# Kernel tuning notes

Hardware: AMD Instinct MI355X
Metric: run time of the kernel (lower is better)

## Reference

```python
import jax, jax.numpy as jnp
import numpy as np

H = 1024      # hidden_size
F = 1024      # intermediate_size
E = 8         # num_experts
K = 2         # num_experts_per_tok
B, S = 1, 2048


def setup_inputs() -> dict:
    key = jax.random.key(0)
    ks = jax.random.split(key, 8)
    s = 0.02
    return {
        "hidden_states": jax.random.normal(ks[0], (B, S, H), jnp.float32),
        "w_gate": jax.random.normal(ks[1], (H, E), jnp.float32) * s,
        "w_gate_proj": jax.random.normal(ks[2], (E, H, F), jnp.float32) * s,   # per-expert gate_proj
        "w_up_proj": jax.random.normal(ks[3], (E, H, F), jnp.float32) * s,     # per-expert up_proj
        "w_down_proj": jax.random.normal(ks[4], (E, F, H), jnp.float32) * s,   # per-expert down_proj
        "w_shared_gate": jax.random.normal(ks[5], (H, F), jnp.float32) * s,
        "w_shared_up": jax.random.normal(ks[6], (H, F), jnp.float32) * s,
        "w_shared_down": jax.random.normal(ks[7], (F, H), jnp.float32) * s,
    }


def reference(hidden_states, w_gate, w_gate_proj, w_up_proj, w_down_proj,
              w_shared_gate, w_shared_up, w_shared_down):
    b, s, h = hidden_states.shape
    x = hidden_states.reshape(-1, h)                       # [T, H]
    t = x.shape[0]

    # --- router ---
    router_logits = x @ w_gate                             # [T, E]
    topk_vals, topk_idx = jax.lax.top_k(router_logits, K)  # [T, K]
    expert_weights = jax.nn.softmax(topk_vals.astype(jnp.float32), axis=-1).astype(x.dtype)

    # dense per-token per-expert combine weight [T, E] (zero where not selected)
    combine = jnp.zeros((t, E), x.dtype).at[jnp.arange(t)[:, None], topk_idx].add(expert_weights)

    # --- all experts as one grouped GEMM (weight-zero experts contribute 0) ---
    g = jnp.einsum('th,ehf->tef', x, w_gate_proj)          # [T, E, F]
    u = jnp.einsum('th,ehf->tef', x, w_up_proj)            # [T, E, F]
    y = jnp.einsum('tef,efh->teh', jax.nn.silu(g) * u, w_down_proj)  # [T, E, H]
    out = jnp.einsum('teh,te->th', y, combine)             # [T, H]

    # --- shared expert ---
    shared = (jax.nn.silu(x @ w_shared_gate) * (x @ w_shared_up)) @ w_shared_down
    out = (out + shared).reshape(b, s, h)

    aux_loss = jnp.float32(0.0)
    return out, aux_loss
```

## Files before the change

kernel.cpp:

```cpp
#include <hip/hip_runtime.h>
#include <hip/hip_bf16.h>
#include <stdint.h>

#define HDIM 1024
#define FDIM 1024
#define TTOK 2048
#define CAP  2048
#define MSZ  (1024*1024)

typedef __attribute__((ext_vector_type(8))) __bf16 bf16x8;
typedef __attribute__((ext_vector_type(4))) float  f32x4;

static __device__ __forceinline__ unsigned short f2bf(float v) {
  unsigned int u = __float_as_uint(v);
  u += 0x7FFF + ((u >> 16) & 1);
  return (unsigned short)(u >> 16);
}

static __device__ __forceinline__ unsigned pk2(float a, float b) {
  return (unsigned)f2bf(a) | ((unsigned)f2bf(b) << 16);
}

static __device__ __forceinline__ void gload_lds16(const void* g, void* l) {
  __builtin_amdgcn_global_load_lds(
      (const __attribute__((address_space(1))) unsigned int*)g,
      (__attribute__((address_space(3))) unsigned int*)l, 16, 0, 0);
}

__global__ __launch_bounds__(256) void k_prep(
    const float* __restrict__ x, const float* __restrict__ wg,
    const float* __restrict__ wgp, const float* __restrict__ wsg,
    const float* __restrict__ wup, const float* __restrict__ wsu,
    const float* __restrict__ wdp, const float* __restrict__ wsd,
    unsigned short* __restrict__ wB, unsigned short* __restrict__ xb,
    int* __restrict__ counts, int* __restrict__ tok_id, float* __restrict__ tok_w) {
  int b = blockIdx.x;
  int tid = threadIdx.x;
  if (b < 3456) {
    int m = b >> 7;
    int idx = b & 127;
    int rblk = idx >> 3, cblk = idx & 7;
    const float* src;
    if (m < 8)       src = wgp + (size_t)m * MSZ;
    else if (m == 8) src = wsg;
    else if (m < 17) src = wup + (size_t)(m - 9) * MSZ;
    else if (m == 17) src = wsu;
    else if (m < 26) src = wdp + (size_t)(m - 18) * MSZ;
    else             src = wsd;
    unsigned short* dst = wB + (size_t)m * MSZ;
    int rb = rblk << 6;
    int cb = cblk << 7;
    int r0 = (tid & 7) << 3;
    int c0 = (tid >> 3) << 2;
    const float* p0 = src + (size_t)(rb + r0) * 1024 + cb + c0;
    f32x4 v[8];
    #pragma unroll
    for (int i = 0; i < 8; i++) {
      asm volatile("global_load_dwordx4 %0, %1, off"
                   : "=&v"(v[i])
                   : "v"(p0 + (size_t)i * 1024));
    }
    asm volatile("s_waitcnt vmcnt(0)" ::: "memory");
    __builtin_amdgcn_sched_barrier(0);
    #pragma unroll
    for (int j = 0; j < 4; j++) {
      uint4 o;
      o.x = pk2(v[0][j], v[1][j]);
      o.y = pk2(v[2][j], v[3][j]);
      o.z = pk2(v[4][j], v[5][j]);
      o.w = pk2(v[6][j], v[7][j]);
      *(uint4*)(dst + (size_t)(cb + c0 + j) * 1024 + rb + r0) = o;
    }
  } else if (b < 3456 + 1024) {
    int i = (b - 3456) * 256 + tid;
    const float4* in4 = (const float4*)x;
    float4 f0 = in4[i * 2], f1 = in4[i * 2 + 1];
    uint4 v;
    v.x = pk2(f0.x, f0.y); v.y = pk2(f0.z, f0.w);
    v.z = pk2(f1.x, f1.y); v.w = pk2(f1.z, f1.w);
    *((uint4*)(xb + (size_t)i * 8)) = v;
    if (i < TTOK) { tok_id[8 * CAP + i] = i; tok_w[8 * CAP + i] = 1.0f; }
    if (i == 0) counts[8] = TTOK;
  } else {
    int t = ((b - 4480) << 2) + (tid >> 6);
    int L = tid & 63;
    const float* xr = x + (size_t)t * HDIM;
    float acc[8] = {0, 0, 0, 0, 0, 0, 0, 0};
    for (int h = L; h < HDIM; h += 64) {
      float xv = xr[h];
      const float* wr = wg + h * 8;
      #pragma unroll
      for (int e = 0; e < 8; e++) acc[e] += xv * wr[e];
    }
    #pragma unroll
    for (int e = 0; e < 8; e++) {
      float v = acc[e];
      for (int off = 32; off > 0; off >>= 1) v += __shfl_xor(v, off);
      acc[e] = v;
    }
    if (L == 0) {
      int i1 = 0; float v1 = acc[0];
      #pragma unroll
      for (int e = 1; e < 8; e++) if (acc[e] > v1) { v1 = acc[e]; i1 = e; }
      int i2 = -1; float v2 = -1e30f;
      #pragma unroll
      for (int e = 0; e < 8; e++) if (e != i1 && acc[e] > v2) { v2 = acc[e]; i2 = e; }
      float ex = __expf(v2 - v1);
      float w1 = 1.f / (1.f + ex);
      float w2 = 1.f - w1;
      int p1 = atomicAdd(&counts[i1], 1);
      tok_id[i1 * CAP + p1] = t; tok_w[i1 * CAP + p1] = w1;
      int p2 = atomicAdd(&counts[i2], 1);
      tok_id[i2 * CAP + p2] = t; tok_w[i2 * CAP + p2] = w2;
    }
  }
}


__global__ __launch_bounds__(256, 4) void k_gemm1(
    const unsigned short* __restrict__ xb, const unsigned short* __restrict__ wB,
    const int* __restrict__ counts, const int* __restrict__ tok_id,
    unsigned short* __restrict__ actb) {
  int lin = blockIdx.x;
  int e = lin >> 8;
  int r9 = lin & 255;
  int nbi = (r9 & 7) | ((r9 >> 7) << 3);
  int mi  = (r9 >> 3) & 15;
  int Ne = (e == 8) ? TTOK : counts[e];
  int rb = mi << 7;
  if (rb >= Ne) return;
  int nb = nbi << 6;
  const unsigned short* wg = wB + (size_t)e * MSZ;
  const unsigned short* wu = wB + (size_t)(9 + e) * MSZ;
  __shared__ __align__(16) unsigned short As[128 * 64];
  __shared__ __align__(16) unsigned short Bgs[64 * 64];
  __shared__ __align__(16) unsigned short Bus[64 * 64];
  int tid = threadIdx.x;
  int w = tid >> 6, L = tid & 63;
  int quad = L >> 4, lane15 = L & 15;
  int wr = w >> 1, wc = w & 1;
  int l7 = lane15 & 7;
  int sw8 = ((L & 7) ^ (L >> 3)) << 3;
  const int* tlist = tok_id + e * CAP + rb;
  int trow[4];
  #pragma unroll
  for (int r = 0; r < 4; r++) {
    int row = (w << 5) + (r << 3) + (L >> 3);
    trow[r] = (rb + row < Ne) ? tlist[row] : 0;
  }
  f32x4 accg[4][2], accu[4][2];
  #pragma unroll
  for (int mt = 0; mt < 4; mt++)
    #pragma unroll
    for (int nt = 0; nt < 2; nt++) {
      accg[mt][nt] = (f32x4){0.f, 0.f, 0.f, 0.f};
      accu[mt][nt] = (f32x4){0.f, 0.f, 0.f, 0.f};
    }
  for (int it = 0; it < 16; it++) {
    int k0 = it << 6;
    #pragma unroll
    for (int r = 0; r < 4; r++)
      gload_lds16(xb + (size_t)trow[r] * 1024 + k0 + sw8, As + ((w << 2) + r) * 512);
    #pragma unroll
    for (int r = 0; r < 2; r++) {
      int fr = (((w << 1) + r) << 3) + (L >> 3);
      size_t go = (size_t)(nb + fr) * 1024 + k0 + sw8;
      gload_lds16(wg + go, Bgs + ((w << 1) + r) * 512);
      gload_lds16(wu + go, Bus + ((w << 1) + r) * 512);
    }
    __syncthreads();
    #pragma unroll
    for (int s = 0; s < 2; s++) {
      bf16x8 a[4], bg[2], bu[2];
      int ch = (s << 2) + quad;
      int po = ((ch ^ l7) << 3);
      #pragma unroll
      for (int mt = 0; mt < 4; mt++)
        a[mt] = *(const bf16x8*)(As + (((wr << 6) + (mt << 4) + lane15) << 6) + po);
      #pragma unroll
      for (int nt = 0; nt < 2; nt++) {
        int rrow = ((wc << 5) + (nt << 4) + lane15) << 6;
        bg[nt] = *(const bf16x8*)(Bgs + rrow + po);
        bu[nt] = *(const bf16x8*)(Bus + rrow + po);
      }
      #pragma unroll
      for (int mt = 0; mt < 4; mt++)
        #pragma unroll
        for (int nt = 0; nt < 2; nt++) {
          accg[mt][nt] = __builtin_amdgcn_mfma_f32_16x16x32_bf16(a[mt], bg[nt], accg[mt][nt], 0, 0, 0);
          accu[mt][nt] = __builtin_amdgcn_mfma_f32_16x16x32_bf16(a[mt], bu[nt], accu[mt][nt], 0, 0, 0);
        }
    }
    __syncthreads();
  }
  #pragma unroll
  for (int mt = 0; mt < 4; mt++)
    #pragma unroll
    for (int nt = 0; nt < 2; nt++)
      #pragma unroll
      for (int g = 0; g < 4; g++) {
        int r = (wr << 6) + (mt << 4) + (quad << 2) + g;
        if (rb + r < Ne) {
          float gv = accg[mt][nt][g], uv = accu[mt][nt][g];
          float av = gv / (1.f + __expf(-gv)) * uv;
          int f = nb + (wc << 5) + (nt << 4) + lane15;
          actb[(size_t)(e * CAP + rb + r) * 1024 + f] = f2bf(av);
        }
      }
}

__global__ __launch_bounds__(256, 4) void k_gemm2(
    const unsigned short* __restrict__ actb, const unsigned short* __restrict__ wB,
    const int* __restrict__ counts, const int* __restrict__ tok_id,
    const float* __restrict__ tok_w, float* __restrict__ out) {
  int lin = blockIdx.x;
  int e = lin >> 7;
  int r8 = lin & 127;
  int nbi = r8 & 7;
  int mi  = r8 >> 3;
  int Ne = (e == 8) ? TTOK : counts[e];
  int rb = mi << 7;
  if (rb >= Ne) return;
  int nb = nbi << 7;
  const unsigned short* wd = wB + (size_t)(18 + e) * MSZ;
  __shared__ __align__(16) unsigned short As[128 * 64];
  __shared__ __align__(16) unsigned short Bs[128 * 64];
  int tid = threadIdx.x;
  int w = tid >> 6, L = tid & 63;
  int quad = L >> 4, lane15 = L & 15;
  int wr = w >> 1, wc = w & 1;
  int l7 = lane15 & 7;
  int sw8 = ((L & 7) ^ (L >> 3)) << 3;
  const unsigned short* arow = actb + (size_t)(e * CAP + rb) * 1024;
  f32x4 acc[4][4];
  #pragma unroll
  for (int mt = 0; mt < 4; mt++)
    #pragma unroll
    for (int nt = 0; nt < 4; nt++) acc[mt][nt] = (f32x4){0.f, 0.f, 0.f, 0.f};
  for (int it = 0; it < 16; it++) {
    int k0 = it << 6;
    #pragma unroll
    for (int r = 0; r < 4; r++) {
      int row = (w << 5) + (r << 3) + (L >> 3);
      gload_lds16(arow + (size_t)row * 1024 + k0 + sw8, As + ((w << 2) + r) * 512);
      gload_lds16(wd + (size_t)(nb + row) * 1024 + k0 + sw8, Bs + ((w << 2) + r) * 512);
    }
    __syncthreads();
    #pragma unroll
    for (int s = 0; s < 2; s++) {
      bf16x8 a[4], b[4];
      int ch = (s << 2) + quad;
      int po = ((ch ^ l7) << 3);
      #pragma unroll
      for (int mt = 0; mt < 4; mt++)
        a[mt] = *(const bf16x8*)(As + (((wr << 6) + (mt << 4) + lane15) << 6) + po);
      #pragma unroll
      for (int nt = 0; nt < 4; nt++)
        b[nt] = *(const bf16x8*)(Bs + (((wc << 6) + (nt << 4) + lane15) << 6) + po);
      #pragma unroll
      for (int mt = 0; mt < 4; mt++)
        #pragma unroll
        for (int nt = 0; nt < 4; nt++)
          acc[mt][nt] = __builtin_amdgcn_mfma_f32_16x16x32_bf16(a[mt], b[nt], acc[mt][nt], 0, 0, 0);
    }
    __syncthreads();
  }
  #pragma unroll
  for (int mt = 0; mt < 4; mt++)
    #pragma unroll
    for (int nt = 0; nt < 4; nt++)
      #pragma unroll
      for (int g = 0; g < 4; g++) {
        int r = (wr << 6) + (mt << 4) + (quad << 2) + g;
        if (rb + r < Ne) {
          int t = tok_id[e * CAP + rb + r];
          float wt = tok_w[e * CAP + rb + r];
          int hc = nb + (wc << 6) + (nt << 4) + lane15;
          atomicAdd(out + (size_t)t * 1024 + hc, acc[mt][nt][g] * wt);
        }
      }
}

extern "C" void kernel_launch(void* const* d_in, const int* in_sizes, int n_in,
                              void* d_out, int out_size, void* d_ws, size_t ws_size,
                              hipStream_t stream) {
  (void)in_sizes; (void)n_in; (void)ws_size;
  const float* x   = (const float*)d_in[0];
  const float* wg  = (const float*)d_in[1];
  const float* wgp = (const float*)d_in[2];
  const float* wup = (const float*)d_in[3];
  const float* wdp = (const float*)d_in[4];
  const float* wsg = (const float*)d_in[5];
  const float* wsu = (const float*)d_in[6];
  const float* wsd = (const float*)d_in[7];
  float* out = (float*)d_out;
  char* ws = (char*)d_ws;
  unsigned short* wB   = (unsigned short*)ws;
  unsigned short* xb   = (unsigned short*)(ws + 56623104);
  unsigned short* actb = (unsigned short*)(ws + 56623104 + 4194304);
  int*   tok_id = (int*)(ws + 56623104 + 4194304 + 37748736);
  float* tok_w  = (float*)(ws + 56623104 + 4194304 + 37748736 + 73728);
  int*   counts = (int*)(ws + 56623104 + 4194304 + 37748736 + 147456);

  hipMemsetAsync(counts, 0, 64, stream);
  hipMemsetAsync(out, 0, (size_t)out_size * 4, stream);
  k_prep<<<4992, 256, 0, stream>>>(x, wg, wgp, wsg, wup, wsu, wdp, wsd,
                                   wB, xb, counts, tok_id, tok_w);
  k_gemm1<<<2304, 256, 0, stream>>>(xb, wB, counts, tok_id, actb);
  k_gemm2<<<1152, 256, 0, stream>>>(actb, wB, counts, tok_id, tok_w, out);
}
```

Measured before the change: 303.4 us.

## Transpose weights through LDS, split prep kernel, and split-K the down-projection GEMM

```diff
diff --git a/kernel.cpp b/kernel.cpp
--- a/kernel.cpp
+++ b/kernel.cpp
@@ -27,52 +27,67 @@
       (__attribute__((address_space(3))) unsigned int*)l, 16, 0, 0);
 }
 
-__global__ __launch_bounds__(256) void k_prep(
-    const float* __restrict__ x, const float* __restrict__ wg,
+__global__ __launch_bounds__(256) void k_tr(
     const float* __restrict__ wgp, const float* __restrict__ wsg,
     const float* __restrict__ wup, const float* __restrict__ wsu,
     const float* __restrict__ wdp, const float* __restrict__ wsd,
-    unsigned short* __restrict__ wB, unsigned short* __restrict__ xb,
+    unsigned short* __restrict__ wB) {
+  int b = blockIdx.x;
+  int m = b >> 6;
+  int idx = b & 63;
+  int rb = (idx >> 3) << 7;
+  int cb = (idx & 7) << 7;
+  const float* src;
+  if (m < 8)       src = wgp + (size_t)m * MSZ;
+  else if (m == 8) src = wsg;
+  else if (m < 17) src = wup + (size_t)(m - 9) * MSZ;
+  else if (m == 17) src = wsu;
+  else if (m < 26) src = wdp + (size_t)(m - 18) * MSZ;
+  else             src = wsd;
+  unsigned short* dst = wB + (size_t)m * MSZ;
+  __shared__ __align__(16) unsigned short T[128 * 128];
+  int tid = threadIdx.x;
+  #pragma unroll
+  for (int i = 0; i < 16; i++) {
+    int g = tid + (i << 8);
+    int r = g >> 5;
+    int f4 = g & 31;
+    float4 v = *(const float4*)(src + (size_t)(rb + r) * 1024 + cb + (f4 << 2));
+    uint2 p;
+    p.x = pk2(v.x, v.y);
+    p.y = pk2(v.z, v.w);
+    int ps = (f4 + ((r >> 3) << 1)) & 31;
+    *(uint2*)(T + r * 128 + (ps << 2)) = p;
+  }
+  __syncthreads();
+  int L = tid & 63, w = tid >> 6;
+  int q = L & 15;
+  int cbase = (w << 2) + (L >> 4);
+  #pragma unroll
+  for (int j = 0; j < 8; j++) {
+    int c = cbase + (j << 4);
+    int ps = ((c >> 2) + (q << 1)) & 31;
+    const unsigned short* p = T + (q << 3) * 128 + (ps << 2) + (c & 3);
+    unsigned short u0 = p[0],       u1 = p[128],      u2 = p[2 * 128],
+                   u3 = p[3 * 128], u4 = p[4 * 128],  u5 = p[5 * 128],
+                   u6 = p[6 * 128], u7 = p[7 * 128];
+    uint4 o;
+    o.x = (unsigned)u0 | ((unsigned)u1 << 16);
+    o.y = (unsigned)u2 | ((unsigned)u3 << 16);
+    o.z = (unsigned)u4 | ((unsigned)u5 << 16);
+    o.w = (unsigned)u6 | ((unsigned)u7 << 16);
+    *(uint4*)(dst + (size_t)(cb + c) * 1024 + rb + (q << 3)) = o;
+  }
+}
+
+__global__ __launch_bounds__(256) void k_misc(
+    const float* __restrict__ x, const float* __restrict__ wg,
+    unsigned short* __restrict__ xb,
     int* __restrict__ counts, int* __restrict__ tok_id, float* __restrict__ tok_w) {
   int b = blockIdx.x;
   int tid = threadIdx.x;
-  if (b < 3456) {
-    int m = b >> 7;
-    int idx = b & 127;
-    int rblk = idx >> 3, cblk = idx & 7;
-    const float* src;
-    if (m < 8)       src = wgp + (size_t)m * MSZ;
-    else if (m == 8) src = wsg;
-    else if (m < 17) src = wup + (size_t)(m - 9) * MSZ;
-    else if (m == 17) src = wsu;
-    else if (m < 26) src = wdp + (size_t)(m - 18) * MSZ;
-    else             src = wsd;
-    unsigned short* dst = wB + (size_t)m * MSZ;
-    int rb = rblk << 6;
-    int cb = cblk << 7;
-    int r0 = (tid & 7) << 3;
-    int c0 = (tid >> 3) << 2;
-    const float* p0 = src + (size_t)(rb + r0) * 1024 + cb + c0;
-    f32x4 v[8];
-    #pragma unroll
-    for (int i = 0; i < 8; i++) {
-      asm volatile("global_load_dwordx4 %0, %1, off"
-                   : "=&v"(v[i])
-                   : "v"(p0 + (size_t)i * 1024));
-    }
-    asm volatile("s_waitcnt vmcnt(0)" ::: "memory");
-    __builtin_amdgcn_sched_barrier(0);
-    #pragma unroll
-    for (int j = 0; j < 4; j++) {
-      uint4 o;
-      o.x = pk2(v[0][j], v[1][j]);
-      o.y = pk2(v[2][j], v[3][j]);
-      o.z = pk2(v[4][j], v[5][j]);
-      o.w = pk2(v[6][j], v[7][j]);
-      *(uint4*)(dst + (size_t)(cb + c0 + j) * 1024 + rb + r0) = o;
-    }
-  } else if (b < 3456 + 1024) {
-    int i = (b - 3456) * 256 + tid;
+  if (b < 1024) {
+    int i = b * 256 + tid;
     const float4* in4 = (const float4*)x;
     float4 f0 = in4[i * 2], f1 = in4[i * 2 + 1];
     uint4 v;
@@ -82,7 +97,7 @@
     if (i < TTOK) { tok_id[8 * CAP + i] = i; tok_w[8 * CAP + i] = 1.0f; }
     if (i == 0) counts[8] = TTOK;
   } else {
-    int t = ((b - 4480) << 2) + (tid >> 6);
+    int t = ((b - 1024) << 2) + (tid >> 6);
     int L = tid & 63;
     const float* xr = x + (size_t)t * HDIM;
     float acc[8] = {0, 0, 0, 0, 0, 0, 0, 0};
@@ -214,10 +229,11 @@
     const int* __restrict__ counts, const int* __restrict__ tok_id,
     const float* __restrict__ tok_w, float* __restrict__ out) {
   int lin = blockIdx.x;
-  int e = lin >> 7;
-  int r8 = lin & 127;
+  int e = lin >> 8;
+  int r8 = lin & 255;
   int nbi = r8 & 7;
-  int mi  = r8 >> 3;
+  int mi  = (r8 >> 3) & 15;
+  int ks  = r8 >> 7;
   int Ne = (e == 8) ? TTOK : counts[e];
   int rb = mi << 7;
   if (rb >= Ne) return;
@@ -237,7 +253,7 @@
   for (int mt = 0; mt < 4; mt++)
     #pragma unroll
     for (int nt = 0; nt < 4; nt++) acc[mt][nt] = (f32x4){0.f, 0.f, 0.f, 0.f};
-  for (int it = 0; it < 16; it++) {
+  for (int it = ks << 3; it < (ks << 3) + 8; it++) {
     int k0 = it << 6;
     #pragma unroll
     for (int r = 0; r < 4; r++) {
@@ -304,8 +320,8 @@
 
   hipMemsetAsync(counts, 0, 64, stream);
   hipMemsetAsync(out, 0, (size_t)out_size * 4, stream);
-  k_prep<<<4992, 256, 0, stream>>>(x, wg, wgp, wsg, wup, wsu, wdp, wsd,
-                                   wB, xb, counts, tok_id, tok_w);
+  k_tr<<<1728, 256, 0, stream>>>(wgp, wsg, wup, wsu, wdp, wsd, wB);
+  k_misc<<<1536, 256, 0, stream>>>(x, wg, xb, counts, tok_id, tok_w);
   k_gemm1<<<2304, 256, 0, stream>>>(xb, wB, counts, tok_id, actb);
-  k_gemm2<<<1152, 256, 0, stream>>>(actb, wB, counts, tok_id, tok_w, out);
-}
+  k_gemm2<<<2304, 256, 0, stream>>>(actb, wB, counts, tok_id, tok_w, out);
+}
```

Measured after the change: 318.5 us. 4.9% more time.
